# Performance work log

Hardware: AMD Instinct MI355X
Metric: run time of the kernel (lower is better)

## Reference

```python
import jax, jax.numpy as jnp
import numpy as np

D = 256       # dim_in
HID = 256     # hidden_dim
L = 4         # memory_bank_len
H = 8         # n_heads
HD = D // H   # head dim
N = 100000    # number of tracks
EPS = 1e-5


def _layer_norm(x, g, b):
    mu = jnp.mean(x, axis=-1, keepdims=True)
    var = jnp.mean(jnp.square(x - mu), axis=-1, keepdims=True)
    return (x - mu) * jax.lax.rsqrt(var + EPS) * g + b


def setup_inputs() -> dict:
    key = jax.random.key(0)
    ks = jax.random.split(key, 16)
    s = 0.02
    inp = {
        "output_embedding": jax.random.normal(ks[0], (N, D), jnp.float32),
        "scores": jax.random.normal(ks[1], (N,), jnp.float32),
        "mem_bank": jax.random.normal(ks[2], (N, L, D), jnp.float32),
        "mem_padding_mask": jax.random.bernoulli(ks[3], 0.5, (N, L)),
        # learned parameters (PyTorch Linear convention: y = x @ W.T + b)
        "save_proj_w": jax.random.normal(ks[4], (D, D), jnp.float32) * s,
        "save_proj_b": jnp.zeros((D,), jnp.float32),
        "in_proj_w": jax.random.normal(ks[5], (3 * D, D), jnp.float32) * s,
        "in_proj_b": jnp.zeros((3 * D,), jnp.float32),
        "out_proj_w": jax.random.normal(ks[6], (D, D), jnp.float32) * s,
        "out_proj_b": jnp.zeros((D,), jnp.float32),
        "fc1_w": jax.random.normal(ks[7], (HID, D), jnp.float32) * s,
        "fc1_b": jnp.zeros((HID,), jnp.float32),
        "fc2_w": jax.random.normal(ks[8], (D, HID), jnp.float32) * s,
        "fc2_b": jnp.zeros((D,), jnp.float32),
        "ln1_g": jnp.ones((D,), jnp.float32),
        "ln1_b": jnp.zeros((D,), jnp.float32),
        "ln2_g": jnp.ones((D,), jnp.float32),
        "ln2_b": jnp.zeros((D,), jnp.float32),
    }
    return inp


def reference(output_embedding, scores, mem_bank, mem_padding_mask,
              save_proj_w, save_proj_b, in_proj_w, in_proj_b,
              out_proj_w, out_proj_b, fc1_w, fc1_b, fc2_w, fc2_b,
              ln1_g, ln1_b, ln2_g, ln2_b):
    n, d = output_embedding.shape
    # valid tracks: last memory slot is not padding
    valid = ~mem_padding_mask[:, -1]                       # [N]
    # for invalid rows, disable padding so softmax stays finite (result discarded)
    kpm = jnp.where(valid[:, None], mem_padding_mask, False)  # [N, L]

    # --- tiny MHA: query = own embedding (len 1), keys/values = mem bank (len L) ---
    q = output_embedding @ in_proj_w[:d].T + in_proj_b[:d]            # [N, D]
    k = mem_bank @ in_proj_w[d:2 * d].T + in_proj_b[d:2 * d]          # [N, L, D]
    v = mem_bank @ in_proj_w[2 * d:].T + in_proj_b[2 * d:]            # [N, L, D]
    qh = q.reshape(n, H, HD)
    kh = k.reshape(n, L, H, HD)
    vh = v.reshape(n, L, H, HD)
    logits = jnp.einsum('nhd,nlhd->nhl', qh, kh) / jnp.sqrt(jnp.asarray(HD, q.dtype))
    logits = jnp.where(kpm[:, None, :], jnp.asarray(-1e9, logits.dtype), logits)
    attn = jax.nn.softmax(logits, axis=-1)                            # [N, H, L]
    ctx = jnp.einsum('nhl,nlhd->nhd', attn, vh).reshape(n, d)
    attn_out = ctx @ out_proj_w.T + out_proj_b

    # --- residual + norm + FFN + norm ---
    e = _layer_norm(output_embedding + attn_out, ln1_g, ln1_b)
    e2 = jax.nn.relu(e @ fc1_w.T + fc1_b) @ fc2_w.T + fc2_b
    e = _layer_norm(e + e2, ln2_g, ln2_b)

    # scatter back only into valid rows
    new_emb = jnp.where(valid[:, None], e, output_embedding)

    # --- update (training branch: saved where scores > 0) ---
    saved = scores > 0                                               # [N]
    save_embed = new_emb @ save_proj_w.T + save_proj_b               # [N, D]
    shifted_bank = jnp.concatenate([mem_bank[:, 1:], save_embed[:, None]], axis=1)
    new_bank = jnp.where(saved[:, None, None], shifted_bank, mem_bank)
    shifted_mask = jnp.concatenate(
        [mem_padding_mask[:, 1:], jnp.zeros((n, 1), bool)], axis=1)
    new_mask = jnp.where(saved[:, None], shifted_mask, mem_padding_mask)
    return new_emb, new_bank, new_mask
```

## Files before the change

kernel.cpp:

```cpp
#include <hip/hip_runtime.h>
#include <hip/hip_bf16.h>
#include <stdint.h>

#define DD 256
#define LL 4
#define HH 8

#define BM 128
#define BN 128
#define BK 32
#define LDA 40
#define CSTR 136

typedef __bf16 bf16_t;
typedef bf16_t bf16x8 __attribute__((ext_vector_type(8)));
typedef float f32x4 __attribute__((ext_vector_type(4)));

__device__ __forceinline__ ushort f2bf(float f) {
  union { float f; uint32_t u; } v; v.f = f;
  uint32_t r = v.u + 0x7FFFu + ((v.u >> 16) & 1u);
  return (ushort)(r >> 16);
}
__device__ __forceinline__ float bf2f(ushort u) {
  union { uint32_t u; float f; } v; v.u = ((uint32_t)u) << 16;
  return v.f;
}
__device__ __forceinline__ bool mval(const void* m, int fmt, size_t idx) {
  if (fmt == 1) return ((const uint8_t*)m)[idx] != 0;
  if (fmt == 2) return ((const float*)m)[idx] != 0.0f;
  return ((const int*)m)[idx] != 0;
}

__global__ void detect_mask_k(const uint8_t* m, int* flag) {
  if (threadIdx.x == 0 && blockIdx.x == 0) {
    bool anybig = false, anyoff = false;
    for (int i = 0; i < 256; i++) {
      uint8_t v = m[i];
      if (v > 1) anybig = true;
      if ((i & 3) && v) anyoff = true;
    }
    *flag = anybig ? 2 : (anyoff ? 1 : 0);
  }
}

__global__ void cast_w_k(const float* __restrict__ ipw, const float* __restrict__ opw,
                         const float* __restrict__ f1w, const float* __restrict__ f2w,
                         const float* __restrict__ svw, ushort* __restrict__ W) {
  int i = blockIdx.x * 256 + threadIdx.x;
  if (i >= 458752) return;
  float v;
  if (i < 196608) v = ipw[i];
  else if (i < 262144) v = opw[i - 196608];
  else if (i < 327680) v = f1w[i - 262144];
  else if (i < 393216) v = f2w[i - 327680];
  else v = svw[i - 393216];
  W[i] = f2bf(v);
}

template<int ABF16, int EPI>
__global__ __launch_bounds__(256, 2)
void gemm_k(const void* __restrict__ Aptr, const ushort* __restrict__ Bw,
            const float* __restrict__ bias, void* __restrict__ Cout, int M,
            const ushort* __restrict__ qbuf, const float* __restrict__ attn,
            const float* __restrict__ scores, float* __restrict__ bank_out,
            float* __restrict__ logits_out, int relu_flag, int n_tracks) {
  extern __shared__ char smem[];
  ushort* Asm = (ushort*)smem;
  ushort* Bsm = Asm + BM * LDA;
  ushort* csubh = (ushort*)smem;

  const int mt = blockIdx.x, nt = blockIdx.y;
  const int tid = threadIdx.x;
  const int wave = tid >> 6, lane = tid & 63;
  const int wm = wave >> 1, wn = wave & 1;
  const int llo = lane & 15, lhi = lane >> 4;
  const int row0 = mt * BM;

  f32x4 acc[4][4];
#pragma unroll
  for (int i = 0; i < 4; i++)
#pragma unroll
    for (int j = 0; j < 4; j++) {
      f32x4 z = {0.0f, 0.0f, 0.0f, 0.0f};
      acc[i][j] = z;
    }

  const int ar = tid >> 1;
  const int acb = (tid & 1) * 16;

  for (int k0 = 0; k0 < DD; k0 += BK) {
    {
      ushort tmp[16];
      int gr = row0 + ar;
      if (ABF16) {
        if (gr < M) {
          const uint4* p = (const uint4*)((const ushort*)Aptr + (size_t)gr * DD + k0 + acb);
          *(uint4*)(tmp) = p[0];
          *(uint4*)(tmp + 8) = p[1];
        } else {
#pragma unroll
          for (int i = 0; i < 16; i++) tmp[i] = 0;
        }
      } else {
        if (gr < M) {
          const float4* p = (const float4*)((const float*)Aptr + (size_t)gr * DD + k0 + acb);
          float4 f0 = p[0], f1 = p[1], f2 = p[2], f3 = p[3];
          tmp[0] = f2bf(f0.x); tmp[1] = f2bf(f0.y); tmp[2] = f2bf(f0.z); tmp[3] = f2bf(f0.w);
          tmp[4] = f2bf(f1.x); tmp[5] = f2bf(f1.y); tmp[6] = f2bf(f1.z); tmp[7] = f2bf(f1.w);
          tmp[8] = f2bf(f2.x); tmp[9] = f2bf(f2.y); tmp[10] = f2bf(f2.z); tmp[11] = f2bf(f2.w);
          tmp[12] = f2bf(f3.x); tmp[13] = f2bf(f3.y); tmp[14] = f2bf(f3.z); tmp[15] = f2bf(f3.w);
        } else {
#pragma unroll
          for (int i = 0; i < 16; i++) tmp[i] = 0;
        }
      }
      ushort* dst = Asm + ar * LDA + acb;
      *(uint4*)dst = *(uint4*)tmp;
      *(uint4*)(dst + 8) = *(uint4*)(tmp + 8);
    }
    if (tid < BN) {
      const ushort* src = Bw + (size_t)(nt * BN + tid) * DD + k0;
      ushort* dst = Bsm + tid * LDA;
      *(uint4*)(dst)      = *(const uint4*)(src);
      *(uint4*)(dst + 8)  = *(const uint4*)(src + 8);
      *(uint4*)(dst + 16) = *(const uint4*)(src + 16);
      *(uint4*)(dst + 24) = *(const uint4*)(src + 24);
    }
    __syncthreads();
    bf16x8 af[4], bfr[4];
#pragma unroll
    for (int i = 0; i < 4; i++)
      af[i] = *(const bf16x8*)(Asm + (wm * 64 + i * 16 + llo) * LDA + lhi * 8);
#pragma unroll
    for (int j = 0; j < 4; j++)
      bfr[j] = *(const bf16x8*)(Bsm + (wn * 64 + j * 16 + llo) * LDA + lhi * 8);
#pragma unroll
    for (int i = 0; i < 4; i++)
#pragma unroll
      for (int j = 0; j < 4; j++)
        acc[i][j] = __builtin_amdgcn_mfma_f32_16x16x32_bf16(af[i], bfr[j], acc[i][j], 0, 0, 0);
    __syncthreads();
  }

  if (EPI == 0) {
    ushort* C = (ushort*)Cout;
#pragma unroll
    for (int i = 0; i < 4; i++)
#pragma unroll
      for (int j = 0; j < 4; j++)
#pragma unroll
        for (int r = 0; r < 4; r++) {
          int rl = wm * 64 + i * 16 + lhi * 4 + r;
          int gr = row0 + rl;
          if (gr < M) {
            int gc = nt * BN + wn * 64 + j * 16 + llo;
            float v = acc[i][j][r] + bias[gc];
            if (relu_flag) v = fmaxf(v, 0.0f);
            C[(size_t)gr * DD + gc] = f2bf(v);
          }
        }
  } else if (EPI == 3) {
#pragma unroll
    for (int i = 0; i < 4; i++)
#pragma unroll
      for (int j = 0; j < 4; j++)
#pragma unroll
        for (int r = 0; r < 4; r++) {
          int rl = wm * 64 + i * 16 + lhi * 4 + r;
          int gr = row0 + rl;
          if (gr < M && scores[gr] > 0.0f) {
            int gc = nt * BN + wn * 64 + j * 16 + llo;
            bank_out[(size_t)gr * 1024 + 768 + gc] = acc[i][j][r] + bias[gc];
          }
        }
  } else {
#pragma unroll
    for (int i = 0; i < 4; i++)
#pragma unroll
      for (int j = 0; j < 4; j++)
#pragma unroll
        for (int r = 0; r < 4; r++) {
          int rl = wm * 64 + i * 16 + lhi * 4 + r;
          int cl = wn * 64 + j * 16 + llo;
          int gc = nt * BN + cl;
          csubh[rl * CSTR + cl] = f2bf(acc[i][j][r] + bias[gc]);
        }
    __syncthreads();
    if (EPI == 1) {
      for (int idx = tid; idx < 512; idx += 256) {
        int trk = idx >> 4;
        int hh = (idx >> 2) & 3;
        int l = idx & 3;
        int trkg = (row0 >> 2) + trk;
        if (trkg < n_tracks) {
          const ushort* qrow = qbuf + (size_t)trkg * DD + nt * BN + hh * 32;
          float dot = 0.0f;
#pragma unroll
          for (int j2 = 0; j2 < 32; j2++)
            dot += bf2f(csubh[(trk * 4 + l) * CSTR + hh * 32 + j2]) * bf2f(qrow[j2]);
          logits_out[(size_t)trkg * 32 + (size_t)(nt * 4 + hh) * 4 + l] = dot * 0.17677669529663687f;
        }
      }
    } else {
      for (int idx = tid; idx < 32 * BN; idx += 256) {
        int trk = idx >> 7, cl = idx & 127;
        int trkg = (row0 >> 2) + trk;
        if (trkg < n_tracks) {
          int gc = nt * BN + cl;
          const float* at = attn + (size_t)trkg * 32 + (size_t)(gc >> 5) * 4;
          float v = at[0] * bf2f(csubh[(trk * 4 + 0) * CSTR + cl])
                  + at[1] * bf2f(csubh[(trk * 4 + 1) * CSTR + cl])
                  + at[2] * bf2f(csubh[(trk * 4 + 2) * CSTR + cl])
                  + at[3] * bf2f(csubh[(trk * 4 + 3) * CSTR + cl]);
          ((ushort*)Cout)[(size_t)trkg * DD + gc] = f2bf(v);
        }
      }
    }
  }
}

__global__ void softmax_k(float* __restrict__ logits, const void* __restrict__ mask,
                          const int* __restrict__ flag, int N) {
  int t = blockIdx.x * 256 + threadIdx.x;
  if (t >= N * HH) return;
  int n = t >> 3, h = t & 7;
  int fmt = *flag;
  bool valid = !mval(mask, fmt, (size_t)n * 4 + 3);
  float* p = logits + (size_t)n * 32 + h * 4;
  float lg[4];
  float mx = -3.0e38f;
#pragma unroll
  for (int l = 0; l < 4; l++) {
    lg[l] = p[l];
    if (valid && mval(mask, fmt, (size_t)n * 4 + l)) lg[l] = -1.0e9f;
    mx = fmaxf(mx, lg[l]);
  }
  float sum = 0.0f;
#pragma unroll
  for (int l = 0; l < 4; l++) { lg[l] = expf(lg[l] - mx); sum += lg[l]; }
  float inv = 1.0f / sum;
#pragma unroll
  for (int l = 0; l < 4; l++) p[l] = lg[l] * inv;
}

__global__ __launch_bounds__(256)
void ln1_k(const float* __restrict__ emb, const ushort* __restrict__ ao,
           const float* __restrict__ g, const float* __restrict__ b,
           ushort* __restrict__ eout, int N) {
  int row = blockIdx.x * 4 + (threadIdx.x >> 6);
  if (row >= N) return;
  int lane = threadIdx.x & 63;
  int c = lane * 4;
  float4 xe = *(const float4*)(emb + (size_t)row * DD + c);
  ushort4 xa = *(const ushort4*)(ao + (size_t)row * DD + c);
  float x0 = xe.x + bf2f(xa.x), x1 = xe.y + bf2f(xa.y);
  float x2 = xe.z + bf2f(xa.z), x3 = xe.w + bf2f(xa.w);
  float s = x0 + x1 + x2 + x3;
  float s2 = x0 * x0 + x1 * x1 + x2 * x2 + x3 * x3;
  for (int off = 1; off < 64; off <<= 1) {
    s += __shfl_xor(s, off);
    s2 += __shfl_xor(s2, off);
  }
  float mu = s * (1.0f / 256.0f);
  float var = s2 * (1.0f / 256.0f) - mu * mu;
  float rs = rsqrtf(var + 1e-5f);
  float4 gv = *(const float4*)(g + c);
  float4 bv = *(const float4*)(b + c);
  ushort4 r;
  r.x = f2bf((x0 - mu) * rs * gv.x + bv.x);
  r.y = f2bf((x1 - mu) * rs * gv.y + bv.y);
  r.z = f2bf((x2 - mu) * rs * gv.z + bv.z);
  r.w = f2bf((x3 - mu) * rs * gv.w + bv.w);
  *(ushort4*)(eout + (size_t)row * DD + c) = r;
}

__global__ __launch_bounds__(256)
void ln2_k(const float* __restrict__ emb, const ushort* __restrict__ e,
           const ushort* __restrict__ f, const float* __restrict__ g,
           const float* __restrict__ b, const void* __restrict__ mask,
           const int* __restrict__ flag, float* __restrict__ out_emb, int N) {
  int row = blockIdx.x * 4 + (threadIdx.x >> 6);
  if (row >= N) return;
  int lane = threadIdx.x & 63;
  int c = lane * 4;
  int fmt = *flag;
  bool valid = !mval(mask, fmt, (size_t)row * 4 + 3);
  ushort4 xe = *(const ushort4*)(e + (size_t)row * DD + c);
  ushort4 xf = *(const ushort4*)(f + (size_t)row * DD + c);
  float x0 = bf2f(xe.x) + bf2f(xf.x), x1 = bf2f(xe.y) + bf2f(xf.y);
  float x2 = bf2f(xe.z) + bf2f(xf.z), x3 = bf2f(xe.w) + bf2f(xf.w);
  float s = x0 + x1 + x2 + x3;
  float s2 = x0 * x0 + x1 * x1 + x2 * x2 + x3 * x3;
  for (int off = 1; off < 64; off <<= 1) {
    s += __shfl_xor(s, off);
    s2 += __shfl_xor(s2, off);
  }
  float mu = s * (1.0f / 256.0f);
  float var = s2 * (1.0f / 256.0f) - mu * mu;
  float rs = rsqrtf(var + 1e-5f);
  float4 gv = *(const float4*)(g + c);
  float4 bv = *(const float4*)(b + c);
  float4 o;
  if (valid) {
    o.x = (x0 - mu) * rs * gv.x + bv.x;
    o.y = (x1 - mu) * rs * gv.y + bv.y;
    o.z = (x2 - mu) * rs * gv.z + bv.z;
    o.w = (x3 - mu) * rs * gv.w + bv.w;
  } else {
    o = *(const float4*)(emb + (size_t)row * DD + c);
  }
  *(float4*)(out_emb + (size_t)row * DD + c) = o;
}

__global__ void bank_k(const float* __restrict__ memb, const float* __restrict__ scores,
                       const void* __restrict__ mask, const int* __restrict__ flag,
                       float* __restrict__ out_bank, float* __restrict__ out_mask, int N) {
  int n = blockIdx.x;
  if (n >= N) return;
  int tid = threadIdx.x;
  int l = tid >> 6, c4 = tid & 63;
  bool saved = scores[n] > 0.0f;
  const float4* mb = (const float4*)(memb + (size_t)n * 1024);
  float4* ob = (float4*)(out_bank + (size_t)n * 1024);
  if (!(saved && l == 3)) {
    int ls = saved ? l + 1 : l;
    ob[l * 64 + c4] = mb[ls * 64 + c4];
  }
  if (tid == 0) {
    int fmt = *flag;
#pragma unroll
    for (int ll2 = 0; ll2 < 4; ll2++) {
      bool mv = saved ? (ll2 < 3 ? mval(mask, fmt, (size_t)n * 4 + ll2 + 1) : false)
                      : mval(mask, fmt, (size_t)n * 4 + ll2);
      out_mask[(size_t)n * 4 + ll2] = mv ? 1.0f : 0.0f;
    }
  }
}

extern "C" void kernel_launch(void* const* d_in, const int* in_sizes, int n_in,
                              void* d_out, int out_size, void* d_ws, size_t ws_size,
                              hipStream_t stream) {
  const float* emb = (const float*)d_in[0];
  const float* scores = (const float*)d_in[1];
  const float* memb = (const float*)d_in[2];
  const void* mask = d_in[3];
  const float* svw = (const float*)d_in[4];
  const float* svb = (const float*)d_in[5];
  const float* ipw = (const float*)d_in[6];
  const float* ipb = (const float*)d_in[7];
  const float* opw = (const float*)d_in[8];
  const float* opb = (const float*)d_in[9];
  const float* f1w = (const float*)d_in[10];
  const float* f1b = (const float*)d_in[11];
  const float* f2w = (const float*)d_in[12];
  const float* f2b = (const float*)d_in[13];
  const float* g1 = (const float*)d_in[14];
  const float* b1 = (const float*)d_in[15];
  const float* g2 = (const float*)d_in[16];
  const float* b2 = (const float*)d_in[17];

  const int N = in_sizes[1];

  float* out = (float*)d_out;
  float* out_emb = out;
  float* out_bank = out + (size_t)N * DD;
  float* out_mask = out + (size_t)N * DD + (size_t)N * LL * DD;

  char* ws = (char*)d_ws;
  ushort* W = (ushort*)ws;
  int* flag = (int*)(ws + 917504);
  float* logits = (float*)(ws + 1048576);
  size_t o = 1048576 + (size_t)N * 32 * 4;
  o = (o + 255) & ~(size_t)255;
  ushort* bufQ = (ushort*)(ws + o); o += (size_t)N * DD * 2;
  ushort* bufC = (ushort*)(ws + o); o += (size_t)N * DD * 2;
  ushort* bufE = (ushort*)(ws + o); o += (size_t)N * DD * 2;
  ushort* bufA = (ushort*)(ws + o); o += (size_t)N * DD * 2;

  cast_w_k<<<(458752 + 255) / 256, 256, 0, stream>>>(ipw, opw, f1w, f2w, svw, W);
  detect_mask_k<<<1, 64, 0, stream>>>((const uint8_t*)mask, flag);

  const int mtN = (N + BM - 1) / BM;
  const int mtKV = (N * LL + BM - 1) / BM;
  const dim3 blk(256);
  const size_t SM_PLAIN = (size_t)(BM + BN) * LDA * 2;
  const size_t SM_EPI   = (size_t)128 * CSTR * 2;

  gemm_k<0, 0><<<dim3(mtN, 2), blk, SM_PLAIN, stream>>>(emb, W, ipb, bufQ, N,
      nullptr, nullptr, nullptr, nullptr, nullptr, 0, N);
  gemm_k<0, 1><<<dim3(mtKV, 2), blk, SM_EPI, stream>>>(memb, W + 65536, ipb + 256, nullptr, N * LL,
      bufQ, nullptr, nullptr, nullptr, logits, 0, N);
  softmax_k<<<(N * HH + 255) / 256, 256, 0, stream>>>(logits, mask, flag, N);
  gemm_k<0, 2><<<dim3(mtKV, 2), blk, SM_EPI, stream>>>(memb, W + 131072, ipb + 512, bufC, N * LL,
      nullptr, logits, nullptr, nullptr, nullptr, 0, N);
  gemm_k<1, 0><<<dim3(mtN, 2), blk, SM_PLAIN, stream>>>(bufC, W + 196608, opb, bufA, N,
      nullptr, nullptr, nullptr, nullptr, nullptr, 0, N);
  ln1_k<<<(N + 3) / 4, 256, 0, stream>>>(emb, bufA, g1, b1, bufE, N);
  gemm_k<1, 0><<<dim3(mtN, 2), blk, SM_PLAIN, stream>>>(bufE, W + 262144, f1b, bufQ, N,
      nullptr, nullptr, nullptr, nullptr, nullptr, 1, N);
  gemm_k<1, 0><<<dim3(mtN, 2), blk, SM_PLAIN, stream>>>(bufQ, W + 327680, f2b, bufC, N,
      nullptr, nullptr, nullptr, nullptr, nullptr, 0, N);
  ln2_k<<<(N + 3) / 4, 256, 0, stream>>>(emb, bufE, bufC, g2, b2, mask, flag, out_emb, N);
  gemm_k<0, 3><<<dim3(mtN, 2), blk, SM_PLAIN, stream>>>(out_emb, W + 393216, svb, nullptr, N,
      nullptr, nullptr, scores, out_bank, nullptr, 0, N);
  bank_k<<<N, 256, 0, stream>>>(memb, scores, mask, flag, out_bank, out_mask, N);
}
```

Measured before the change: 1.598 ms.

## Fuse K/V projection, attention softmax and bank shift into one kernel

Replaces the separate K-projection GEMM, softmax kernel and V-projection GEMM with one 512-thread kernel. It computes K and V for a 128-row tile of the memory bank in a single pass (N=512), then does the q·k logits, masked softmax and attention-weighted V reduction in shared memory and registers. The bank-shift and mask copy is folded into the same kernel, so mem_bank (about 400MB in fp32) is read once instead of three times and the logits round trip through global memory goes away. The grid for the remaining GEMMs is transposed so N-tiles vary fastest, and static shared memory replaces dynamic. The costs are higher register pressure from the 4x8 accumulator tile and a softmax stage that runs on only half the waves.

```diff
diff --git a/kernel.cpp b/kernel.cpp
--- a/kernel.cpp
+++ b/kernel.cpp
@@ -1,5 +1,4 @@
 #include <hip/hip_runtime.h>
-#include <hip/hip_bf16.h>
 #include <stdint.h>
 
 #define DD 256
@@ -10,7 +9,8 @@
 #define BN 128
 #define BK 32
 #define LDA 40
-#define CSTR 136
+#define KSTR 136
+#define QSTR 264
 
 typedef __bf16 bf16_t;
 typedef bf16_t bf16x8 __attribute__((ext_vector_type(8)));
@@ -61,15 +61,12 @@
 __global__ __launch_bounds__(256, 2)
 void gemm_k(const void* __restrict__ Aptr, const ushort* __restrict__ Bw,
             const float* __restrict__ bias, void* __restrict__ Cout, int M,
-            const ushort* __restrict__ qbuf, const float* __restrict__ attn,
             const float* __restrict__ scores, float* __restrict__ bank_out,
-            float* __restrict__ logits_out, int relu_flag, int n_tracks) {
-  extern __shared__ char smem[];
-  ushort* Asm = (ushort*)smem;
-  ushort* Bsm = Asm + BM * LDA;
-  ushort* csubh = (ushort*)smem;
-
-  const int mt = blockIdx.x, nt = blockIdx.y;
+            int relu_flag) {
+  __shared__ ushort Asm[BM * LDA];
+  __shared__ ushort Bsm[BN * LDA];
+
+  const int nt = blockIdx.x, mt = blockIdx.y;
   const int tid = threadIdx.x;
   const int wave = tid >> 6, lane = tid & 63;
   const int wm = wave >> 1, wn = wave & 1;
@@ -159,7 +156,7 @@
             C[(size_t)gr * DD + gc] = f2bf(v);
           }
         }
-  } else if (EPI == 3) {
+  } else {
 #pragma unroll
     for (int i = 0; i < 4; i++)
 #pragma unroll
@@ -173,74 +170,198 @@
             bank_out[(size_t)gr * 1024 + 768 + gc] = acc[i][j][r] + bias[gc];
           }
         }
-  } else {
-#pragma unroll
-    for (int i = 0; i < 4; i++)
-#pragma unroll
-      for (int j = 0; j < 4; j++)
+  }
+}
+
+__global__ __launch_bounds__(512, 2)
+void kv_attn_k(const float* __restrict__ memb, const ushort* __restrict__ Wkv,
+               const float* __restrict__ ipb, const ushort* __restrict__ qbuf,
+               ushort* __restrict__ ctx_out, const void* __restrict__ mask,
+               const int* __restrict__ flag, const float* __restrict__ scores,
+               float* __restrict__ out_bank, float* __restrict__ out_mask, int N) {
+  extern __shared__ char smem[];
+  ushort* Asm = (ushort*)smem;
+  ushort* Bsm = Asm + 128 * LDA;
+  ushort* Ksm = (ushort*)smem;
+  ushort* qsm = Ksm + 128 * KSTR;
+  float* attn_s = (float*)(qsm + 32 * QSTR);
+
+  const int mt = blockIdx.x;
+  const int tid = threadIdx.x;
+  const int wave = tid >> 6, lane = tid & 63;
+  const int wm = wave >> 2, wn = wave & 3;
+  const int llo = lane & 15, lhi = lane >> 4;
+  const int row0 = mt * 128;
+  const int trk0 = mt * 32;
+  const int M = N * 4;
+
+  f32x4 acc[4][8];
+#pragma unroll
+  for (int i = 0; i < 4; i++)
+#pragma unroll
+    for (int j = 0; j < 8; j++) {
+      f32x4 z = {0.0f, 0.0f, 0.0f, 0.0f};
+      acc[i][j] = z;
+    }
+
+  const int ar = tid >> 2;
+  const int acb = (tid & 3) * 8;
+
+  for (int k0 = 0; k0 < DD; k0 += BK) {
+    {
+      ushort tmp[8];
+      int gr = row0 + ar;
+      if (gr < M) {
+        const float4* p = (const float4*)(memb + (size_t)gr * DD + k0 + acb);
+        float4 f0 = p[0], f1 = p[1];
+        tmp[0] = f2bf(f0.x); tmp[1] = f2bf(f0.y); tmp[2] = f2bf(f0.z); tmp[3] = f2bf(f0.w);
+        tmp[4] = f2bf(f1.x); tmp[5] = f2bf(f1.y); tmp[6] = f2bf(f1.z); tmp[7] = f2bf(f1.w);
+      } else {
+#pragma unroll
+        for (int i = 0; i < 8; i++) tmp[i] = 0;
+      }
+      *(uint4*)(Asm + ar * LDA + acb) = *(uint4*)tmp;
+    }
+    {
+      const ushort* src = Wkv + (size_t)tid * DD + k0;
+      ushort* dst = Bsm + tid * LDA;
+      *(uint4*)(dst)      = *(const uint4*)(src);
+      *(uint4*)(dst + 8)  = *(const uint4*)(src + 8);
+      *(uint4*)(dst + 16) = *(const uint4*)(src + 16);
+      *(uint4*)(dst + 24) = *(const uint4*)(src + 24);
+    }
+    __syncthreads();
+    bf16x8 af[4], bfr[8];
+#pragma unroll
+    for (int i = 0; i < 4; i++)
+      af[i] = *(const bf16x8*)(Asm + (wm * 64 + i * 16 + llo) * LDA + lhi * 8);
+#pragma unroll
+    for (int j = 0; j < 8; j++)
+      bfr[j] = *(const bf16x8*)(Bsm + (wn * 128 + j * 16 + llo) * LDA + lhi * 8);
+#pragma unroll
+    for (int i = 0; i < 4; i++)
+#pragma unroll
+      for (int j = 0; j < 8; j++)
+        acc[i][j] = __builtin_amdgcn_mfma_f32_16x16x32_bf16(af[i], bfr[j], acc[i][j], 0, 0, 0);
+    __syncthreads();
+  }
+
+  const int fmt = *flag;
+
+  if (wn < 2) {
+#pragma unroll
+    for (int j = 0; j < 8; j++) {
+      int cl = wn * 128 + j * 16 + llo;
+      float kb = ipb[256 + cl];
+#pragma unroll
+      for (int i = 0; i < 4; i++)
 #pragma unroll
         for (int r = 0; r < 4; r++) {
           int rl = wm * 64 + i * 16 + lhi * 4 + r;
-          int cl = wn * 64 + j * 16 + llo;
-          int gc = nt * BN + cl;
-          csubh[rl * CSTR + cl] = f2bf(acc[i][j][r] + bias[gc]);
-        }
-    __syncthreads();
-    if (EPI == 1) {
-      for (int idx = tid; idx < 512; idx += 256) {
-        int trk = idx >> 4;
-        int hh = (idx >> 2) & 3;
-        int l = idx & 3;
-        int trkg = (row0 >> 2) + trk;
-        if (trkg < n_tracks) {
-          const ushort* qrow = qbuf + (size_t)trkg * DD + nt * BN + hh * 32;
-          float dot = 0.0f;
-#pragma unroll
-          for (int j2 = 0; j2 < 32; j2++)
-            dot += bf2f(csubh[(trk * 4 + l) * CSTR + hh * 32 + j2]) * bf2f(qrow[j2]);
-          logits_out[(size_t)trkg * 32 + (size_t)(nt * 4 + hh) * 4 + l] = dot * 0.17677669529663687f;
-        }
-      }
+          Ksm[rl * KSTR + cl] = f2bf(acc[i][j][r] + kb);
+        }
+    }
+  } else {
+    int vt = (wm * 2 + (wn - 2)) * 64 + lane;
+    int trk = vt >> 3;
+    int c0 = (vt & 7) * 32;
+    int trkg = trk0 + trk;
+    ushort* dst = qsm + trk * QSTR + c0;
+    if (trkg < N) {
+      const uint4* src = (const uint4*)(qbuf + (size_t)trkg * DD + c0);
+      ((uint4*)dst)[0] = src[0];
+      ((uint4*)dst)[1] = src[1];
+      ((uint4*)dst)[2] = src[2];
+      ((uint4*)dst)[3] = src[3];
     } else {
-      for (int idx = tid; idx < 32 * BN; idx += 256) {
-        int trk = idx >> 7, cl = idx & 127;
-        int trkg = (row0 >> 2) + trk;
-        if (trkg < n_tracks) {
-          int gc = nt * BN + cl;
-          const float* at = attn + (size_t)trkg * 32 + (size_t)(gc >> 5) * 4;
-          float v = at[0] * bf2f(csubh[(trk * 4 + 0) * CSTR + cl])
-                  + at[1] * bf2f(csubh[(trk * 4 + 1) * CSTR + cl])
-                  + at[2] * bf2f(csubh[(trk * 4 + 2) * CSTR + cl])
-                  + at[3] * bf2f(csubh[(trk * 4 + 3) * CSTR + cl]);
-          ((ushort*)Cout)[(size_t)trkg * DD + gc] = f2bf(v);
-        }
-      }
-    }
-  }
-}
-
-__global__ void softmax_k(float* __restrict__ logits, const void* __restrict__ mask,
-                          const int* __restrict__ flag, int N) {
-  int t = blockIdx.x * 256 + threadIdx.x;
-  if (t >= N * HH) return;
-  int n = t >> 3, h = t & 7;
-  int fmt = *flag;
-  bool valid = !mval(mask, fmt, (size_t)n * 4 + 3);
-  float* p = logits + (size_t)n * 32 + h * 4;
-  float lg[4];
-  float mx = -3.0e38f;
-#pragma unroll
-  for (int l = 0; l < 4; l++) {
-    lg[l] = p[l];
-    if (valid && mval(mask, fmt, (size_t)n * 4 + l)) lg[l] = -1.0e9f;
-    mx = fmaxf(mx, lg[l]);
-  }
-  float sum = 0.0f;
-#pragma unroll
-  for (int l = 0; l < 4; l++) { lg[l] = expf(lg[l] - mx); sum += lg[l]; }
-  float inv = 1.0f / sum;
-#pragma unroll
-  for (int l = 0; l < 4; l++) p[l] = lg[l] * inv;
+      uint4 z = {0, 0, 0, 0};
+      ((uint4*)dst)[0] = z; ((uint4*)dst)[1] = z;
+      ((uint4*)dst)[2] = z; ((uint4*)dst)[3] = z;
+    }
+  }
+  __syncthreads();
+
+  if (wn < 2) {
+    int vt = (wm * 2 + wn) * 64 + lane;
+    int trk = vt >> 3, hh = vt & 7;
+    int trkg = trk0 + trk;
+    if (trkg < N) {
+      float qv[32];
+      const bf16x8* qp8 = (const bf16x8*)(qsm + trk * QSTR + hh * 32);
+#pragma unroll
+      for (int c8 = 0; c8 < 4; c8++) {
+        bf16x8 q8 = qp8[c8];
+#pragma unroll
+        for (int e = 0; e < 8; e++) qv[c8 * 8 + e] = (float)q8[e];
+      }
+      bool valid = !mval(mask, fmt, (size_t)trkg * 4 + 3);
+      float lg[4];
+      float mx = -3.0e38f;
+#pragma unroll
+      for (int l = 0; l < 4; l++) {
+        const bf16x8* kp8 = (const bf16x8*)(Ksm + (trk * 4 + l) * KSTR + hh * 32);
+        float dot = 0.0f;
+#pragma unroll
+        for (int c8 = 0; c8 < 4; c8++) {
+          bf16x8 k8 = kp8[c8];
+#pragma unroll
+          for (int e = 0; e < 8; e++) dot += qv[c8 * 8 + e] * (float)k8[e];
+        }
+        dot *= 0.17677669529663687f;
+        if (valid && mval(mask, fmt, (size_t)trkg * 4 + l)) dot = -1.0e9f;
+        lg[l] = dot;
+        mx = fmaxf(mx, dot);
+      }
+      float sum = 0.0f;
+#pragma unroll
+      for (int l = 0; l < 4; l++) { lg[l] = expf(lg[l] - mx); sum += lg[l]; }
+      float inv = 1.0f / sum;
+#pragma unroll
+      for (int l = 0; l < 4; l++) attn_s[trk * 32 + hh * 4 + l] = lg[l] * inv;
+    }
+  } else {
+    int vt = (wm * 2 + (wn - 2)) * 64 + lane;
+    int rl = vt >> 1;
+    int chunk = (vt & 1) * 128;
+    int trk = rl >> 2, l = rl & 3;
+    int trkg = trk0 + trk;
+    if (trkg < N) {
+      bool saved = scores[trkg] > 0.0f;
+      if (chunk == 0) {
+        bool mv = saved ? (l < 3 ? mval(mask, fmt, (size_t)trkg * 4 + l + 1) : false)
+                        : mval(mask, fmt, (size_t)trkg * 4 + l);
+        out_mask[(size_t)trkg * 4 + l] = mv ? 1.0f : 0.0f;
+      }
+      if (!(saved && l == 3)) {
+        int ls = saved ? l + 1 : l;
+        const float4* s = (const float4*)(memb + ((size_t)trkg * 4 + ls) * DD + chunk);
+        float4* d = (float4*)(out_bank + ((size_t)trkg * 4 + l) * DD + chunk);
+#pragma unroll 8
+        for (int q = 0; q < 32; q++) d[q] = s[q];
+      }
+    }
+  }
+  __syncthreads();
+
+  if (wn >= 2) {
+#pragma unroll
+    for (int j = 0; j < 8; j++) {
+      int vcol = (wn - 2) * 128 + j * 16 + llo;
+      float vb = ipb[512 + vcol];
+      int h4 = (vcol >> 5) * 4;
+#pragma unroll
+      for (int i = 0; i < 4; i++) {
+        int t = wm * 16 + i * 4 + lhi;
+        int trkg = trk0 + t;
+        if (trkg < N) {
+          const float* at = attn_s + t * 32 + h4;
+          float v = at[0] * acc[i][j][0] + at[1] * acc[i][j][1]
+                  + at[2] * acc[i][j][2] + at[3] * acc[i][j][3] + vb;
+          ctx_out[(size_t)trkg * DD + vcol] = f2bf(v);
+        }
+      }
+    }
+  }
 }
 
 __global__ __launch_bounds__(256)
@@ -310,31 +431,6 @@
     o = *(const float4*)(emb + (size_t)row * DD + c);
   }
   *(float4*)(out_emb + (size_t)row * DD + c) = o;
-}
-
-__global__ void bank_k(const float* __restrict__ memb, const float* __restrict__ scores,
-                       const void* __restrict__ mask, const int* __restrict__ flag,
-                       float* __restrict__ out_bank, float* __restrict__ out_mask, int N) {
-  int n = blockIdx.x;
-  if (n >= N) return;
-  int tid = threadIdx.x;
-  int l = tid >> 6, c4 = tid & 63;
-  bool saved = scores[n] > 0.0f;
-  const float4* mb = (const float4*)(memb + (size_t)n * 1024);
-  float4* ob = (float4*)(out_bank + (size_t)n * 1024);
-  if (!(saved && l == 3)) {
-    int ls = saved ? l + 1 : l;
-    ob[l * 64 + c4] = mb[ls * 64 + c4];
-  }
-  if (tid == 0) {
-    int fmt = *flag;
-#pragma unroll
-    for (int ll2 = 0; ll2 < 4; ll2++) {
-      bool mv = saved ? (ll2 < 3 ? mval(mask, fmt, (size_t)n * 4 + ll2 + 1) : false)
-                      : mval(mask, fmt, (size_t)n * 4 + ll2);
-      out_mask[(size_t)n * 4 + ll2] = mv ? 1.0f : 0.0f;
-    }
-  }
 }
 
 extern "C" void kernel_launch(void* const* d_in, const int* in_sizes, int n_in,
@@ -369,9 +465,7 @@
   char* ws = (char*)d_ws;
   ushort* W = (ushort*)ws;
   int* flag = (int*)(ws + 917504);
-  float* logits = (float*)(ws + 1048576);
-  size_t o = 1048576 + (size_t)N * 32 * 4;
-  o = (o + 255) & ~(size_t)255;
+  size_t o = 1048576;
   ushort* bufQ = (ushort*)(ws + o); o += (size_t)N * DD * 2;
   ushort* bufC = (ushort*)(ws + o); o += (size_t)N * DD * 2;
   ushort* bufE = (ushort*)(ws + o); o += (size_t)N * DD * 2;
@@ -381,27 +475,22 @@
   detect_mask_k<<<1, 64, 0, stream>>>((const uint8_t*)mask, flag);
 
   const int mtN = (N + BM - 1) / BM;
-  const int mtKV = (N * LL + BM - 1) / BM;
+  const int mtKV = (N * LL + 127) / 128;
   const dim3 blk(256);
-  const size_t SM_PLAIN = (size_t)(BM + BN) * LDA * 2;
-  const size_t SM_EPI   = (size_t)128 * CSTR * 2;
-
-  gemm_k<0, 0><<<dim3(mtN, 2), blk, SM_PLAIN, stream>>>(emb, W, ipb, bufQ, N,
-      nullptr, nullptr, nullptr, nullptr, nullptr, 0, N);
-  gemm_k<0, 1><<<dim3(mtKV, 2), blk, SM_EPI, stream>>>(memb, W + 65536, ipb + 256, nullptr, N * LL,
-      bufQ, nullptr, nullptr, nullptr, logits, 0, N);
-  softmax_k<<<(N * HH + 255) / 256, 256, 0, stream>>>(logits, mask, flag, N);
-  gemm_k<0, 2><<<dim3(mtKV, 2), blk, SM_EPI, stream>>>(memb, W + 131072, ipb + 512, bufC, N * LL,
-      nullptr, logits, nullptr, nullptr, nullptr, 0, N);
-  gemm_k<1, 0><<<dim3(mtN, 2), blk, SM_PLAIN, stream>>>(bufC, W + 196608, opb, bufA, N,
-      nullptr, nullptr, nullptr, nullptr, nullptr, 0, N);
+  const size_t SM_KV = (size_t)128 * KSTR * 2 + (size_t)32 * QSTR * 2 + 32 * 32 * 4;
+
+  gemm_k<0, 0><<<dim3(2, mtN), blk, 0, stream>>>(emb, W, ipb, bufQ, N,
+      nullptr, nullptr, 0);
+  kv_attn_k<<<dim3(mtKV), dim3(512), SM_KV, stream>>>(memb, W + 65536, ipb, bufQ,
+      bufC, mask, flag, scores, out_bank, out_mask, N);
+  gemm_k<1, 0><<<dim3(2, mtN), blk, 0, stream>>>(bufC, W + 196608, opb, bufA, N,
+      nullptr, nullptr, 0);
   ln1_k<<<(N + 3) / 4, 256, 0, stream>>>(emb, bufA, g1, b1, bufE, N);
-  gemm_k<1, 0><<<dim3(mtN, 2), blk, SM_PLAIN, stream>>>(bufE, W + 262144, f1b, bufQ, N,
-      nullptr, nullptr, nullptr, nullptr, nullptr, 1, N);
-  gemm_k<1, 0><<<dim3(mtN, 2), blk, SM_PLAIN, stream>>>(bufQ, W + 327680, f2b, bufC, N,
-      nullptr, nullptr, nullptr, nullptr, nullptr, 0, N);
+  gemm_k<1, 0><<<dim3(2, mtN), blk, 0, stream>>>(bufE, W + 262144, f1b, bufQ, N,
+      nullptr, nullptr, 1);
+  gemm_k<1, 0><<<dim3(2, mtN), blk, 0, stream>>>(bufQ, W + 327680, f2b, bufC, N,
+      nullptr, nullptr, 0);
   ln2_k<<<(N + 3) / 4, 256, 0, stream>>>(emb, bufE, bufC, g2, b2, mask, flag, out_emb, N);
-  gemm_k<0, 3><<<dim3(mtN, 2), blk, SM_PLAIN, stream>>>(out_emb, W + 393216, svb, nullptr, N,
-      nullptr, nullptr, scores, out_bank, nullptr, 0, N);
-  bank_k<<<N, 256, 0, stream>>>(memb, scores, mask, flag, out_bank, out_mask, N);
-}
+  gemm_k<0, 3><<<dim3(2, mtN), blk, 0, stream>>>(out_emb, W + 393216, svb, nullptr, N,
+      scores, out_bank, 0);
+}
```

New measurement: 1.494 ms. -6.5%, faster.
